# Performance work log

Measured on AMD Instinct MI355X. Metric: run time of the kernel, lower is better.

Reference implementation:

```python
import jax, jax.numpy as jnp
import numpy as np

B_, L_, H_, N_ = 8, 1024, 1024, 64

def setup_inputs() -> dict:
    key = jax.random.key(0)
    k1, k2, k3, k4 = jax.random.split(key, 4)
    return {
        "samples": jax.random.normal(k1, (B_, L_, 3 * H_), dtype=jnp.float32),
        "label_one_hot": jax.random.uniform(k2, (B_, L_, N_), dtype=jnp.float32),
        "predict": jax.random.normal(k3, (B_, L_, N_), dtype=jnp.float32),
        "W": jax.random.normal(k4, (H_, 3 * H_), dtype=jnp.float32) * (1.0 / np.sqrt(3 * H_)),
        "b_proj": jnp.zeros((H_,), dtype=jnp.float32),
    }

def reference(samples, label_one_hot, predict, W, b_proj):
    # projection: Linear(3H -> H)
    s = jnp.einsum("blk,hk->blh", samples, W) + b_proj          # [b,L,H]
    # dense similarity graph with diagonal masked out, row-softmax
    graph = jnp.einsum("blh,bmh->blm", s, s)                     # [b,L,L]
    L = graph.shape[1]
    eye = jnp.eye(L, dtype=graph.dtype)
    A = jax.nn.softmax(graph - 1e5 * eye, axis=-1)               # [b,L,L]
    # centered masked labels
    sup = label_one_hot
    row_has = (jnp.sum(sup, axis=-1) > 0.5).astype(sup.dtype)    # [b,L]
    total = jnp.sum(row_has, axis=-1)[:, None]                   # [b,1]
    avg = (jnp.sum(sup, axis=-2) / total)[:, None, :]            # [b,1,N]
    B0 = (sup - avg) * row_has[..., None]                        # [b,L,N]
    # diagonal inverse-degree scaling (elementwise, no dense diag matmul)
    d = 1.0 / (jnp.sum(A, axis=-1) + 1e-10)                      # [b,L]
    P = d[:, :, None] * jnp.swapaxes(A, -1, -2)                  # [b,L,L]
    Db = d[:, :, None] * B0                                      # [b,L,N]
    # 6-step power-iteration scan with residual injection at t==3
    ut = jnp.zeros_like(B0)
    for t in range(1, 7):
        ut = jnp.einsum("blm,bmn->bln", P, ut) + Db
        if t == 3:
            ut = ut + predict  # dropout is identity in eval mode
    return ut

if __name__ == "__main__":
    out = reference(**setup_inputs())
    print(out.shape, out.dtype)
```

## Files before the change

### kernel.cpp

```cpp
#include <hip/hip_runtime.h>


typedef _Float16 f16_t;
typedef f16_t f16x4 __attribute__((ext_vector_type(4)));
typedef f16_t f16x8 __attribute__((ext_vector_type(8)));
typedef float floatx4 __attribute__((ext_vector_type(4)));

__device__ __forceinline__ void async_copy16(const void* g, void* l) {
  __builtin_amdgcn_global_load_lds(
      (const __attribute__((address_space(1))) void*)g,
      (__attribute__((address_space(3))) void*)l, 16, 0, 0);
}

__device__ __forceinline__ f16_t hi_of(float x) { return (f16_t)x; }
__device__ __forceinline__ f16_t lo_of(float x, f16_t h) {
  return (f16_t)(x - (float)h);
}

__global__ __launch_bounds__(256) void split_kernel(
    const float* __restrict__ x, f16_t* __restrict__ hi,
    f16_t* __restrict__ lo, int n4, float scale)
{
  const int i = blockIdx.x * 256 + threadIdx.x;
  if (i >= n4) return;
  float4 v = ((const float4*)x)[i];
  v.x *= scale; v.y *= scale; v.z *= scale; v.w *= scale;
  f16x4 h, l;
  f16_t h0 = hi_of(v.x); h[0] = h0; l[0] = lo_of(v.x, h0);
  f16_t h1 = hi_of(v.y); h[1] = h1; l[1] = lo_of(v.y, h1);
  f16_t h2 = hi_of(v.z); h[2] = h2; l[2] = lo_of(v.z, h2);
  f16_t h3 = hi_of(v.w); h[3] = h3; l[3] = lo_of(v.w, h3);
  *(f16x4*)(hi + (size_t)i * 4) = h;
  *(f16x4*)(lo + (size_t)i * 4) = l;
}

__global__ __launch_bounds__(256) void cvt16_kernel(
    const float* __restrict__ x, f16_t* __restrict__ y, int n4)
{
  const int i = blockIdx.x * 256 + threadIdx.x;
  if (i >= n4) return;
  const float4 v = ((const float4*)x)[i];
  f16x4 h;
  h[0] = (f16_t)v.x; h[1] = (f16_t)v.y; h[2] = (f16_t)v.z; h[3] = (f16_t)v.w;
  *(f16x4*)(y + (size_t)i * 4) = h;
}

template <int CMODE>
__global__ __launch_bounds__(256) void gemm_mfma(
    const f16_t* __restrict__ AhiG,
    const f16_t* __restrict__ BhiG, const f16_t* __restrict__ BloG,
    const float* __restrict__ bias,
    float* __restrict__ Cf, f16_t* __restrict__ Chi, f16_t* __restrict__ Clo,
    int M, int N, int K, long long sA, long long sB, long long sC, float cscale)
{
  AhiG += (long long)blockIdx.z * sA;
  BhiG += (long long)blockIdx.z * sB;
  BloG += (long long)blockIdx.z * sB;
  if (CMODE == 1) Cf += (long long)blockIdx.z * sC;

  __shared__ __align__(16) f16_t AsHi[128 * 32];
  __shared__ __align__(16) f16_t BsHi[128 * 32];
  __shared__ __align__(16) f16_t BsLo[128 * 32];

  const int tid = threadIdx.x;
  const int lane = tid & 63;
  const int wave = tid >> 6;
  const int wm = wave >> 1, wn = wave & 1;
  const int m0 = blockIdx.y * 128;
  const int n0 = blockIdx.x * 128;

  const int fr = lane & 15;
  const int kg = (lane >> 4) * 8;
  const int aoff = (wm * 64 + fr) * 32 + kg;
  const int boff = (wn * 64 + fr) * 32 + kg;

  floatx4 acc[4][4] = {};

  for (int k0 = 0; k0 < K; k0 += 32) {
    __syncthreads();
#pragma unroll
    for (int it = 0; it < 2; ++it) {
      const int cb = it * 256 + wave * 64;
      const int c = cb + lane;
      const int row = c >> 2, kc = (c & 3) * 8;
      const size_t aoffg = (size_t)(m0 + row) * K + k0 + kc;
      const size_t boffg = (size_t)(n0 + row) * K + k0 + kc;
      async_copy16(AhiG + aoffg, (char*)AsHi + (size_t)cb * 16);
      async_copy16(BhiG + boffg, (char*)BsHi + (size_t)cb * 16);
      async_copy16(BloG + boffg, (char*)BsLo + (size_t)cb * 16);
    }
    __syncthreads();

    f16x8 ah[4], bh[4], bl[4];
#pragma unroll
    for (int t = 0; t < 4; ++t) {
      ah[t] = *(const f16x8*)&AsHi[aoff + t * 512];
      bh[t] = *(const f16x8*)&BsHi[boff + t * 512];
      bl[t] = *(const f16x8*)&BsLo[boff + t * 512];
    }
#pragma unroll
    for (int i = 0; i < 4; ++i)
#pragma unroll
      for (int j = 0; j < 4; ++j) {
        acc[i][j] = __builtin_amdgcn_mfma_f32_16x16x32_f16(ah[i], bh[j], acc[i][j], 0, 0, 0);
        acc[i][j] = __builtin_amdgcn_mfma_f32_16x16x32_f16(ah[i], bl[j], acc[i][j], 0, 0, 0);
      }
  }

  const int mr = (lane >> 4) * 4;
#pragma unroll
  for (int j = 0; j < 4; ++j) {
    const int n = n0 + wn * 64 + j * 16 + fr;
    const float bj = (CMODE == 0) ? bias[n] : 0.f;
#pragma unroll
    for (int i = 0; i < 4; ++i) {
#pragma unroll
      for (int r = 0; r < 4; ++r) {
        const int m = m0 + wm * 64 + i * 16 + mr + r;
        float v = acc[i][j][r];
        if (CMODE == 0) {
          v = v * cscale + bj;
          f16_t h = hi_of(v);
          Chi[(size_t)m * N + n] = h;
          Clo[(size_t)m * N + n] = lo_of(v, h);
        } else {
          if (m == n) v -= 1e5f;
          Cf[(size_t)m * N + n] = v;
        }
      }
    }
  }
}

__global__ __launch_bounds__(256) void rowstats_kernel(
    const float* __restrict__ G, float* __restrict__ mx, float* __restrict__ inv)
{
  __shared__ float red[4];
  const int tid = threadIdx.x;
  const float* g = G + (size_t)blockIdx.x * 1024;
  const float4 v = ((const float4*)g)[tid];

  float m = fmaxf(fmaxf(v.x, v.y), fmaxf(v.z, v.w));
#pragma unroll
  for (int off = 32; off > 0; off >>= 1) m = fmaxf(m, __shfl_down(m, off));
  if ((tid & 63) == 0) red[tid >> 6] = m;
  __syncthreads();
  m = fmaxf(fmaxf(red[0], red[1]), fmaxf(red[2], red[3]));
  __syncthreads();

  float s = __expf(v.x - m) + __expf(v.y - m) + __expf(v.z - m) + __expf(v.w - m);
#pragma unroll
  for (int off = 32; off > 0; off >>= 1) s += __shfl_down(s, off);
  if ((tid & 63) == 0) red[tid >> 6] = s;
  __syncthreads();
  if (tid == 0) {
    mx[blockIdx.x] = m;
    inv[blockIdx.x] = 1.0f / (red[0] + red[1] + red[2] + red[3]);
  }
}

__global__ __launch_bounds__(256) void make_at_kernel(
    const float* __restrict__ G, const float* __restrict__ mx,
    const float* __restrict__ inv, f16_t* __restrict__ At)
{
  const int row = blockIdx.x;
  const int b = row >> 10;
  const int tid = threadIdx.x;
  const float4 g = ((const float4*)(G + (size_t)row * 1024))[tid];
  const float4 m = ((const float4*)(mx + b * 1024))[tid];
  const float4 iv = ((const float4*)(inv + b * 1024))[tid];
  f16x4 o;
  o[0] = (f16_t)(__expf(g.x - m.x) * iv.x);
  o[1] = (f16_t)(__expf(g.y - m.y) * iv.y);
  o[2] = (f16_t)(__expf(g.z - m.z) * iv.z);
  o[3] = (f16_t)(__expf(g.w - m.w) * iv.w);
  *(f16x4*)(At + (size_t)row * 1024 + tid * 4) = o;
}

__global__ __launch_bounds__(1024) void make_db_kernel(
    const float* __restrict__ sup, float* __restrict__ Db)
{
  const int L = 1024, Nn = 64;
  const float* s = sup + (size_t)blockIdx.x * L * Nn;
  float* db = Db + (size_t)blockIdx.x * L * Nn;
  __shared__ float rowhas[1024];
  __shared__ float cpart[1024];
  __shared__ float tpart[16];
  __shared__ float avg[64];
  __shared__ float totalsh;
  const int tid = threadIdx.x;

  const float4* sr = (const float4*)(s + (size_t)tid * 64);
  float ss = 0.f;
#pragma unroll
  for (int i = 0; i < 16; ++i) { const float4 v = sr[i]; ss += (v.x + v.y) + (v.z + v.w); }
  const float rh = (ss > 0.5f) ? 1.f : 0.f;
  rowhas[tid] = rh;
  float t = rh;
#pragma unroll
  for (int off = 32; off > 0; off >>= 1) t += __shfl_down(t, off);
  if ((tid & 63) == 0) tpart[tid >> 6] = t;

  const int n = tid & 63, seg = tid >> 6;
  float cs = 0.f;
  for (int l = seg * 64; l < seg * 64 + 64; ++l) cs += s[(size_t)l * 64 + n];
  cpart[seg * 64 + n] = cs;
  __syncthreads();
  if (tid == 0) { float tt = 0.f; for (int i = 0; i < 16; ++i) tt += tpart[i]; totalsh = tt; }
  __syncthreads();
  if (tid < 64) {
    float a = 0.f;
    for (int i = 0; i < 16; ++i) a += cpart[i * 64 + tid];
    avg[tid] = a / totalsh;
  }
  __syncthreads();

  const float4* s4 = (const float4*)s;
  float4* d4 = (float4*)db;
  for (int i = tid; i < (L * Nn) / 4; i += 1024) {
    float4 v = s4[i];
    const int l = i >> 4;
    const int nb = (i & 15) * 4;
    const float rhl = rowhas[l];
    v.x = (v.x - avg[nb + 0]) * rhl;
    v.y = (v.y - avg[nb + 1]) * rhl;
    v.z = (v.z - avg[nb + 2]) * rhl;
    v.w = (v.w - avg[nb + 3]) * rhl;
    d4[i] = v;
  }
}

__global__ __launch_bounds__(256) void transpose_db_kernel(
    const float* __restrict__ Db, f16_t* __restrict__ DbT)
{
  __shared__ f16_t T[64 * 72];
  const int b = blockIdx.y, l0 = blockIdx.x * 64;
  const int tid = threadIdx.x;
  const float* src = Db + (size_t)b * 1024 * 64;
  f16_t* dst = DbT + (size_t)b * 64 * 1024;
#pragma unroll
  for (int it = 0; it < 4; ++it) {
    const int c = it * 256 + tid;
    const int l = c >> 4, nc = (c & 15) * 4;
    const float4 v = *(const float4*)(src + (size_t)(l0 + l) * 64 + nc);
    T[(nc + 0) * 72 + l] = (f16_t)v.x;
    T[(nc + 1) * 72 + l] = (f16_t)v.y;
    T[(nc + 2) * 72 + l] = (f16_t)v.z;
    T[(nc + 3) * 72 + l] = (f16_t)v.w;
  }
  __syncthreads();
#pragma unroll
  for (int it = 0; it < 2; ++it) {
    const int c = it * 256 + tid;
    const int n = c >> 3, lc = (c & 7) * 8;
    *(f16x8*)(dst + (size_t)n * 1024 + l0 + lc) = *(const f16x8*)&T[n * 72 + lc];
  }
}

__global__ __launch_bounds__(256) void iter_part(
    const f16_t* __restrict__ At, const f16_t* __restrict__ UT,
    float* __restrict__ Part)
{
  const int L = 1024, Nn = 64;
  const int b = blockIdx.y, l0 = blockIdx.x * 64, ks = blockIdx.z;
  At += (size_t)b * L * L;
  UT += (size_t)b * Nn * L;
  Part += (((size_t)ks * 8 + b) * L) * Nn;

  __shared__ __align__(16) f16_t AtS[2 * 64 * 32];
  __shared__ __align__(16) f16_t UtS[2 * 64 * 32];

  const int tid = threadIdx.x;
  const int lane = tid & 63;
  const int wave = tid >> 6;
  const int fr = lane & 15;
  const int kg = (lane >> 4) * 8;

  floatx4 acc[4] = {};

  for (int mi = 0; mi < 4; ++mi) {
    const int m0 = ks * 256 + mi * 64;
    __syncthreads();
#pragma unroll
    for (int it = 0; it < 2; ++it) {
      const int cb = it * 256 + wave * 64;
      const int c = cb + lane;
      const int kk = c >> 8;
      const int row = (c >> 2) & 63;
      const int kc = kk * 32 + (c & 3) * 8;
      async_copy16(At + (size_t)(l0 + row) * L + m0 + kc, (char*)AtS + (size_t)cb * 16);
      async_copy16(UT + (size_t)row * L + m0 + kc, (char*)UtS + (size_t)cb * 16);
    }
    __syncthreads();
#pragma unroll
    for (int kk = 0; kk < 2; ++kk) {
      const f16x8 a = *(const f16x8*)&AtS[kk * 2048 + (wave * 16 + fr) * 32 + kg];
#pragma unroll
      for (int j = 0; j < 4; ++j) {
        const f16x8 bf = *(const f16x8*)&UtS[kk * 2048 + (j * 16 + fr) * 32 + kg];
        acc[j] = __builtin_amdgcn_mfma_f32_16x16x32_f16(a, bf, acc[j], 0, 0, 0);
      }
    }
  }

  const int mr = (lane >> 4) * 4;
#pragma unroll
  for (int j = 0; j < 4; ++j) {
    const int n = j * 16 + fr;
#pragma unroll
    for (int r = 0; r < 4; ++r) {
      const int l = wave * 16 + mr + r;
      Part[(size_t)(l0 + l) * Nn + n] = acc[j][r];
    }
  }
}

template <int PRED, int FINAL>
__global__ __launch_bounds__(256) void iter_fin(
    const float* __restrict__ Part, const float* __restrict__ Db,
    const float* __restrict__ Pred, f16_t* __restrict__ UTn,
    float* __restrict__ OutF)
{
  const int L = 1024, Nn = 64;
  const int b = blockIdx.y, l0 = blockIdx.x * 64;
  const size_t base = ((size_t)b * L + l0) * Nn;
  const size_t ksStride = (size_t)8 * L * Nn;
  Db += base;
  if (PRED) Pred += base;

  __shared__ f16_t OutS[64 * 72];
  const int tid = threadIdx.x;

#pragma unroll
  for (int it = 0; it < 4; ++it) {
    const int idx = it * 256 + tid;
    const int l = idx >> 4, n4 = (idx & 15) * 4;
    const size_t o = (size_t)l * Nn + n4;
    float4 v = *(const float4*)(Part + base + o);
    const float4 p1 = *(const float4*)(Part + base + ksStride + o);
    const float4 p2 = *(const float4*)(Part + base + 2 * ksStride + o);
    const float4 p3 = *(const float4*)(Part + base + 3 * ksStride + o);
    v.x += p1.x; v.y += p1.y; v.z += p1.z; v.w += p1.w;
    v.x += p2.x; v.y += p2.y; v.z += p2.z; v.w += p2.w;
    v.x += p3.x; v.y += p3.y; v.z += p3.z; v.w += p3.w;
    const float4 d = *(const float4*)(Db + o);
    v.x += d.x; v.y += d.y; v.z += d.z; v.w += d.w;
    if (PRED) {
      const float4 p = *(const float4*)(Pred + o);
      v.x += p.x; v.y += p.y; v.z += p.z; v.w += p.w;
    }
    if (FINAL) {
      *(float4*)(OutF + base + o) = v;
    } else {
      OutS[(n4 + 0) * 72 + l] = (f16_t)v.x;
      OutS[(n4 + 1) * 72 + l] = (f16_t)v.y;
      OutS[(n4 + 2) * 72 + l] = (f16_t)v.z;
      OutS[(n4 + 3) * 72 + l] = (f16_t)v.w;
    }
  }
  if (!FINAL) {
    __syncthreads();
    f16_t* dst = UTn + (size_t)b * Nn * L;
#pragma unroll
    for (int it = 0; it < 2; ++it) {
      const int c = it * 256 + tid;
      const int n = c >> 3, lc = (c & 7) * 8;
      *(f16x8*)(dst + (size_t)n * L + l0 + lc) = *(const f16x8*)&OutS[n * 72 + lc];
    }
  }
}

extern "C" void kernel_launch(void* const* d_in, const int* in_sizes, int n_in,
                              void* d_out, int out_size, void* d_ws, size_t ws_size,
                              hipStream_t stream) {
  const float* samples = (const float*)d_in[0];
  const float* label   = (const float*)d_in[1];
  const float* predict = (const float*)d_in[2];
  const float* W       = (const float*)d_in[3];
  const float* bproj   = (const float*)d_in[4];
  float* out = (float*)d_out;

  char* ws = (char*)d_ws;
  f16_t* Whi = (f16_t*)ws;
  f16_t* Wlo = (f16_t*)(ws + 6291456);
  float* mx  = (float*)ws;
  float* inv = (float*)(ws + 32768);
  float* Db  = (float*)(ws + 65536);
  f16_t* DbT = (f16_t*)(ws + 65536 + 2097152);
  f16_t* UTa = (f16_t*)(ws + 65536 + 3145728);
  f16_t* UTb = (f16_t*)(ws + 65536 + 4194304);
  f16_t* SampH = (f16_t*)(ws + 12582912);
  float* G     = (float*)(ws + 12582912);
  f16_t* Shi = (f16_t*)(ws + 62914560);
  f16_t* Slo = (f16_t*)(ws + 62914560 + 16777216);
  f16_t* At  = Shi;
  float* Part = (float*)Slo;

  const long long LH = 1024LL * 1024;
  const long long LL = 1024LL * 1024;

  split_kernel<<<dim3(1024 * 3072 / 4 / 256), 256, 0, stream>>>(
      W, Whi, Wlo, 1024 * 3072 / 4, 32.0f);
  cvt16_kernel<<<dim3(8192 * 3072 / 4 / 256), 256, 0, stream>>>(
      samples, SampH, 8192 * 3072 / 4);

  gemm_mfma<0><<<dim3(8, 64, 1), 256, 0, stream>>>(
      SampH, Whi, Wlo, bproj, nullptr, Shi, Slo,
      8192, 1024, 3072, 0, 0, 0, 1.0f / 32.0f);

  gemm_mfma<1><<<dim3(8, 8, 8), 256, 0, stream>>>(
      Shi, Shi, Slo, nullptr, G, nullptr, nullptr,
      1024, 1024, 1024, LH, LH, LL, 1.0f);

  rowstats_kernel<<<8192, 256, 0, stream>>>(G, mx, inv);
  make_at_kernel<<<8192, 256, 0, stream>>>(G, mx, inv, At);

  make_db_kernel<<<8, 1024, 0, stream>>>(label, Db);
  transpose_db_kernel<<<dim3(16, 8), 256, 0, stream>>>(Db, DbT);

  dim3 gp(16, 8, 4), gf(16, 8);
  iter_part<<<gp, 256, 0, stream>>>(At, DbT, Part);
  iter_fin<0, 0><<<gf, 256, 0, stream>>>(Part, Db, nullptr, UTa, nullptr);
  iter_part<<<gp, 256, 0, stream>>>(At, UTa, Part);
  iter_fin<1, 0><<<gf, 256, 0, stream>>>(Part, Db, predict, UTb, nullptr);
  iter_part<<<gp, 256, 0, stream>>>(At, UTb, Part);
  iter_fin<0, 0><<<gf, 256, 0, stream>>>(Part, Db, nullptr, UTa, nullptr);
  iter_part<<<gp, 256, 0, stream>>>(At, UTa, Part);
  iter_fin<0, 0><<<gf, 256, 0, stream>>>(Part, Db, nullptr, UTb, nullptr);
  iter_part<<<gp, 256, 0, stream>>>(At, UTb, Part);
  iter_fin<0, 1><<<gf, 256, 0, stream>>>(Part, Db, nullptr, nullptr, out);
}
```

Before: 422.4 us.

## Merge prep kernels, widen GEMM K-step to 64, fold Db transpose into make_db

Combines the W split and samples fp16 conversion into one launch, and folds the Db transpose into make_db_kernel, so two kernel launches go away. The MFMA GEMM now loads a K=64 slab per iteration (two 32-wide sub-tiles in LDS), which halves the number of barrier pairs per tile at the cost of more shared memory per block. The fused transpose does strided, uncoalesced reads of the labels from only 8 blocks, which may be slower than the dedicated transpose kernel.

Result: no change. 420.8 us (-0.4%).

```diff
diff --git a/kernel.cpp b/kernel.cpp
--- a/kernel.cpp
+++ b/kernel.cpp
@@ -17,32 +17,29 @@
   return (f16_t)(x - (float)h);
 }
 
-__global__ __launch_bounds__(256) void split_kernel(
-    const float* __restrict__ x, f16_t* __restrict__ hi,
-    f16_t* __restrict__ lo, int n4, float scale)
-{
-  const int i = blockIdx.x * 256 + threadIdx.x;
-  if (i >= n4) return;
-  float4 v = ((const float4*)x)[i];
-  v.x *= scale; v.y *= scale; v.z *= scale; v.w *= scale;
-  f16x4 h, l;
-  f16_t h0 = hi_of(v.x); h[0] = h0; l[0] = lo_of(v.x, h0);
-  f16_t h1 = hi_of(v.y); h[1] = h1; l[1] = lo_of(v.y, h1);
-  f16_t h2 = hi_of(v.z); h[2] = h2; l[2] = lo_of(v.z, h2);
-  f16_t h3 = hi_of(v.w); h[3] = h3; l[3] = lo_of(v.w, h3);
-  *(f16x4*)(hi + (size_t)i * 4) = h;
-  *(f16x4*)(lo + (size_t)i * 4) = l;
-}
-
-__global__ __launch_bounds__(256) void cvt16_kernel(
-    const float* __restrict__ x, f16_t* __restrict__ y, int n4)
-{
-  const int i = blockIdx.x * 256 + threadIdx.x;
-  if (i >= n4) return;
-  const float4 v = ((const float4*)x)[i];
-  f16x4 h;
-  h[0] = (f16_t)v.x; h[1] = (f16_t)v.y; h[2] = (f16_t)v.z; h[3] = (f16_t)v.w;
-  *(f16x4*)(y + (size_t)i * 4) = h;
+__global__ __launch_bounds__(256) void prep_kernel(
+    const float* __restrict__ W, f16_t* __restrict__ Whi, f16_t* __restrict__ Wlo,
+    const float* __restrict__ samples, f16_t* __restrict__ SampH)
+{
+  const int bx = blockIdx.x, tid = threadIdx.x;
+  if (bx < 3072) {
+    const int i = bx * 256 + tid;
+    float4 v = ((const float4*)W)[i];
+    v.x *= 32.f; v.y *= 32.f; v.z *= 32.f; v.w *= 32.f;
+    f16x4 h, l;
+    f16_t h0 = hi_of(v.x); h[0] = h0; l[0] = lo_of(v.x, h0);
+    f16_t h1 = hi_of(v.y); h[1] = h1; l[1] = lo_of(v.y, h1);
+    f16_t h2 = hi_of(v.z); h[2] = h2; l[2] = lo_of(v.z, h2);
+    f16_t h3 = hi_of(v.w); h[3] = h3; l[3] = lo_of(v.w, h3);
+    *(f16x4*)(Whi + (size_t)i * 4) = h;
+    *(f16x4*)(Wlo + (size_t)i * 4) = l;
+  } else {
+    const int i = (bx - 3072) * 256 + tid;
+    const float4 v = ((const float4*)samples)[i];
+    f16x4 h;
+    h[0] = (f16_t)v.x; h[1] = (f16_t)v.y; h[2] = (f16_t)v.z; h[3] = (f16_t)v.w;
+    *(f16x4*)(SampH + (size_t)i * 4) = h;
+  }
 }
 
 template <int CMODE>
@@ -58,9 +55,9 @@
   BloG += (long long)blockIdx.z * sB;
   if (CMODE == 1) Cf += (long long)blockIdx.z * sC;
 
-  __shared__ __align__(16) f16_t AsHi[128 * 32];
-  __shared__ __align__(16) f16_t BsHi[128 * 32];
-  __shared__ __align__(16) f16_t BsLo[128 * 32];
+  __shared__ __align__(16) f16_t AsHi[2 * 128 * 32];
+  __shared__ __align__(16) f16_t BsHi[2 * 128 * 32];
+  __shared__ __align__(16) f16_t BsLo[2 * 128 * 32];
 
   const int tid = threadIdx.x;
   const int lane = tid & 63;
@@ -76,35 +73,40 @@
 
   floatx4 acc[4][4] = {};
 
-  for (int k0 = 0; k0 < K; k0 += 32) {
+  for (int k0 = 0; k0 < K; k0 += 64) {
     __syncthreads();
 #pragma unroll
-    for (int it = 0; it < 2; ++it) {
+    for (int it = 0; it < 4; ++it) {
       const int cb = it * 256 + wave * 64;
       const int c = cb + lane;
-      const int row = c >> 2, kc = (c & 3) * 8;
-      const size_t aoffg = (size_t)(m0 + row) * K + k0 + kc;
-      const size_t boffg = (size_t)(n0 + row) * K + k0 + kc;
-      async_copy16(AhiG + aoffg, (char*)AsHi + (size_t)cb * 16);
-      async_copy16(BhiG + boffg, (char*)BsHi + (size_t)cb * 16);
-      async_copy16(BloG + boffg, (char*)BsLo + (size_t)cb * 16);
+      const int kk = c >> 9;
+      const int row = (c >> 2) & 127;
+      const int kc = kk * 32 + (c & 3) * 8;
+      const size_t ga = (size_t)(m0 + row) * K + k0 + kc;
+      const size_t gb = (size_t)(n0 + row) * K + k0 + kc;
+      async_copy16(AhiG + ga, (char*)AsHi + (size_t)cb * 16);
+      async_copy16(BhiG + gb, (char*)BsHi + (size_t)cb * 16);
+      async_copy16(BloG + gb, (char*)BsLo + (size_t)cb * 16);
     }
     __syncthreads();
 
-    f16x8 ah[4], bh[4], bl[4];
-#pragma unroll
-    for (int t = 0; t < 4; ++t) {
-      ah[t] = *(const f16x8*)&AsHi[aoff + t * 512];
-      bh[t] = *(const f16x8*)&BsHi[boff + t * 512];
-      bl[t] = *(const f16x8*)&BsLo[boff + t * 512];
-    }
-#pragma unroll
-    for (int i = 0; i < 4; ++i)
-#pragma unroll
-      for (int j = 0; j < 4; ++j) {
-        acc[i][j] = __builtin_amdgcn_mfma_f32_16x16x32_f16(ah[i], bh[j], acc[i][j], 0, 0, 0);
-        acc[i][j] = __builtin_amdgcn_mfma_f32_16x16x32_f16(ah[i], bl[j], acc[i][j], 0, 0, 0);
+#pragma unroll
+    for (int kk = 0; kk < 2; ++kk) {
+      f16x8 ah[4], bh[4], bl[4];
+#pragma unroll
+      for (int t = 0; t < 4; ++t) {
+        ah[t] = *(const f16x8*)&AsHi[kk * 4096 + aoff + t * 512];
+        bh[t] = *(const f16x8*)&BsHi[kk * 4096 + boff + t * 512];
+        bl[t] = *(const f16x8*)&BsLo[kk * 4096 + boff + t * 512];
       }
+#pragma unroll
+      for (int i = 0; i < 4; ++i)
+#pragma unroll
+        for (int j = 0; j < 4; ++j) {
+          acc[i][j] = __builtin_amdgcn_mfma_f32_16x16x32_f16(ah[i], bh[j], acc[i][j], 0, 0, 0);
+          acc[i][j] = __builtin_amdgcn_mfma_f32_16x16x32_f16(ah[i], bl[j], acc[i][j], 0, 0, 0);
+        }
+    }
   }
 
   const int mr = (lane >> 4) * 4;
@@ -178,11 +180,12 @@
 }
 
 __global__ __launch_bounds__(1024) void make_db_kernel(
-    const float* __restrict__ sup, float* __restrict__ Db)
+    const float* __restrict__ sup, float* __restrict__ Db, f16_t* __restrict__ DbT)
 {
   const int L = 1024, Nn = 64;
   const float* s = sup + (size_t)blockIdx.x * L * Nn;
   float* db = Db + (size_t)blockIdx.x * L * Nn;
+  f16_t* dbt = DbT + (size_t)blockIdx.x * L * Nn;
   __shared__ float rowhas[1024];
   __shared__ float cpart[1024];
   __shared__ float tpart[16];
@@ -228,32 +231,9 @@
     v.w = (v.w - avg[nb + 3]) * rhl;
     d4[i] = v;
   }
-}
-
-__global__ __launch_bounds__(256) void transpose_db_kernel(
-    const float* __restrict__ Db, f16_t* __restrict__ DbT)
-{
-  __shared__ f16_t T[64 * 72];
-  const int b = blockIdx.y, l0 = blockIdx.x * 64;
-  const int tid = threadIdx.x;
-  const float* src = Db + (size_t)b * 1024 * 64;
-  f16_t* dst = DbT + (size_t)b * 64 * 1024;
-#pragma unroll
-  for (int it = 0; it < 4; ++it) {
-    const int c = it * 256 + tid;
-    const int l = c >> 4, nc = (c & 15) * 4;
-    const float4 v = *(const float4*)(src + (size_t)(l0 + l) * 64 + nc);
-    T[(nc + 0) * 72 + l] = (f16_t)v.x;
-    T[(nc + 1) * 72 + l] = (f16_t)v.y;
-    T[(nc + 2) * 72 + l] = (f16_t)v.z;
-    T[(nc + 3) * 72 + l] = (f16_t)v.w;
-  }
-  __syncthreads();
-#pragma unroll
-  for (int it = 0; it < 2; ++it) {
-    const int c = it * 256 + tid;
-    const int n = c >> 3, lc = (c & 7) * 8;
-    *(f16x8*)(dst + (size_t)n * 1024 + l0 + lc) = *(const f16x8*)&T[n * 72 + lc];
+  for (int i = tid; i < L * Nn; i += 1024) {
+    const int n2 = i >> 10, l2 = i & 1023;
+    dbt[i] = (f16_t)((s[(size_t)l2 * 64 + n2] - avg[n2]) * rowhas[l2]);
   }
 }
 
@@ -399,10 +379,7 @@
   const long long LH = 1024LL * 1024;
   const long long LL = 1024LL * 1024;
 
-  split_kernel<<<dim3(1024 * 3072 / 4 / 256), 256, 0, stream>>>(
-      W, Whi, Wlo, 1024 * 3072 / 4, 32.0f);
-  cvt16_kernel<<<dim3(8192 * 3072 / 4 / 256), 256, 0, stream>>>(
-      samples, SampH, 8192 * 3072 / 4);
+  prep_kernel<<<dim3(27648), 256, 0, stream>>>(W, Whi, Wlo, samples, SampH);
 
   gemm_mfma<0><<<dim3(8, 64, 1), 256, 0, stream>>>(
       SampH, Whi, Wlo, bproj, nullptr, Shi, Slo,
@@ -415,8 +392,7 @@
   rowstats_kernel<<<8192, 256, 0, stream>>>(G, mx, inv);
   make_at_kernel<<<8192, 256, 0, stream>>>(G, mx, inv, At);
 
-  make_db_kernel<<<8, 1024, 0, stream>>>(label, Db);
-  transpose_db_kernel<<<dim3(16, 8), 256, 0, stream>>>(Db, DbT);
+  make_db_kernel<<<8, 1024, 0, stream>>>(label, Db, DbT);
 
   dim3 gp(16, 8, 4), gf(16, 8);
   iter_part<<<gp, 256, 0, stream>>>(At, DbT, Part);
```
